# Kernel tuning notes

Measured on AMD Instinct MI355X. Metric: run time of the kernel, lower is better.

The kernel has to match this reference:

```python
import jax, jax.numpy as jnp
import numpy as np

B, S, TRG, SRC2 = 64, 2048, 512, 1024  # batch, src_len, trg_hidden, 2*src_hidden


def setup_inputs() -> dict:
    key = jax.random.key(0)
    ks = jax.random.split(key, 9)
    return {
        "dehy": jax.random.normal(ks[0], (B, TRG), dtype=jnp.float32),
        "enhy": jax.random.normal(ks[1], (B, S, SRC2), dtype=jnp.float32),
        "past_attn": jax.random.uniform(ks[2], (B, S), dtype=jnp.float32),
        "src_mask": jax.random.randint(ks[3], (B, S), 0, 2, dtype=jnp.int32),
        # parameters (torch Linear: y = x @ W.T + b)
        "W_en": jax.random.normal(ks[4], (TRG, SRC2), dtype=jnp.float32) * 0.02,
        "b_en": jnp.zeros((TRG,), dtype=jnp.float32),
        "W_de": jax.random.normal(ks[5], (TRG, TRG), dtype=jnp.float32) * 0.02,
        "w_cv": jax.random.normal(ks[6], (TRG,), dtype=jnp.float32) * 0.02,   # attn_cv_in: Linear(1, trg)
        "w_warp": jax.random.normal(ks[7], (TRG,), dtype=jnp.float32) * 0.02, # attn_warp_in: Linear(trg, 1)
    }


def reference(dehy, enhy, past_attn, src_mask, W_en, b_en, W_de, w_cv, w_warp):
    # luong_concat score with 'asee' coverage term
    # attn_agg: [B, S, TRG]
    attn_agg = (
        jnp.einsum("bsd,hd->bsh", enhy, W_en) + b_en
        + (dehy @ W_de.T)[:, None, :]
        + past_attn[..., None] * w_cv
    )
    attn_agg = jnp.tanh(attn_agg)
    attn_ee = jnp.einsum("bsh,h->bs", attn_agg, w_warp)  # [B, S]
    # masked_fill(|mask| == 0, -1e20)
    attn_ee = jnp.where(jnp.abs(src_mask) == 0, jnp.float32(-1e20), attn_ee)
    attn = jax.nn.softmax(attn_ee, axis=1)
    c_encoder = jnp.einsum("bs,bsd->bd", attn, enhy)  # [B, SRC2]
    return (c_encoder, attn, attn_ee)
```

## Files before the change

### kernel.cpp

```cpp
#include <hip/hip_runtime.h>
#include <hip/hip_bf16.h>

#define B_   64
#define S_   2048
#define TRG_ 512
#define K_   1024

typedef short short8 __attribute__((ext_vector_type(8)));
typedef short short4v __attribute__((ext_vector_type(4)));
typedef float f32x4  __attribute__((ext_vector_type(4)));
typedef unsigned short us4 __attribute__((ext_vector_type(4)));

__device__ __forceinline__ unsigned short f2bf(float f) {
    union { float f; unsigned int u; } v; v.f = f;
    unsigned int u = v.u;
    unsigned int r = (u + 0x7fffu + ((u >> 16) & 1u)) >> 16;
    return (unsigned short)r;
}

__device__ __forceinline__ short4v cvt4(f32x4 a) {
    union { __hip_bfloat162 h[2]; short4v v; } u;
    u.h[0] = __float22bfloat162_rn(float2{a[0], a[1]});
    u.h[1] = __float22bfloat162_rn(float2{a[2], a[3]});
    return u.v;
}

__global__ void wen_convert_kernel(const float* __restrict__ Wen,
                                   unsigned short* __restrict__ Wbf) {
    int idx = blockIdx.x * 256 + threadIdx.x;
    float4 f = ((const float4*)Wen)[idx];
    us4 o = { f2bf(f.x), f2bf(f.y), f2bf(f.z), f2bf(f.w) };
    ((us4*)Wbf)[idx] = o;
}

__global__ void deproj_kernel(const float* __restrict__ dehy,
                              const float* __restrict__ Wde,
                              const float* __restrict__ ben,
                              float* __restrict__ dp) {
    int b = blockIdx.x >> 1;
    int h = ((blockIdx.x & 1) << 8) + threadIdx.x;
    const float4* dv = (const float4*)(dehy + (size_t)b * TRG_);
    const float4* wv = (const float4*)(Wde + (size_t)h * TRG_);
    float s = ben[h];
    #pragma unroll 4
    for (int t = 0; t < TRG_ / 4; ++t) {
        float4 a = dv[t], w = wv[t];
        s += a.x * w.x + a.y * w.y + a.z * w.z + a.w * w.w;
    }
    dp[b * TRG_ + h] = s;
}

__global__ __launch_bounds__(512, 4) void score_kernel(
    const float* __restrict__ enhy,
    const unsigned short* __restrict__ Wbf,
    const float* __restrict__ dp,
    const float* __restrict__ past_attn,
    const int* __restrict__ src_mask,
    const float* __restrict__ w_cv,
    const float* __restrict__ w_warp,
    float* __restrict__ out_ee)
{
    __shared__ unsigned short Bbuf[512 * 32];
    __shared__ unsigned short Abuf[2][64 * 32];
    __shared__ float red[8][64];

    const int tid  = threadIdx.x;
    const int lane = tid & 63;
    const int w    = tid >> 6;
    const int lj   = lane & 15;
    const int lg   = lane >> 4;
    const int m0   = blockIdx.x * 64;
    const int b    = m0 >> 11;

    const int kx = ((lg ^ ((lj >> 1) & 3)) << 4);

    f32x4 acc[4][4];
    const f32x4 fz = {0.f, 0.f, 0.f, 0.f};
    #pragma unroll
    for (int i = 0; i < 4; ++i)
        #pragma unroll
        for (int j = 0; j < 4; ++j) acc[i][j] = fz;

    const int arow = tid >> 3;
    const int akq  = tid & 7;
    const float* aSrc = enhy + (size_t)(m0 + arow) * K_ + (akq << 2);
    const int aDstByte = arow * 64 + (((akq >> 1) ^ ((arow >> 1) & 3)) << 4) + ((akq & 1) << 3);

    const int brow0 = tid >> 2;
    const int bkc0  = tid & 3;
    const unsigned short* bSrc0 = Wbf + (size_t)brow0 * K_ + ((bkc0 ^ ((brow0 >> 1) & 3)) << 3);
    const int bDst0 = w * 1024;

#define LOADA(R, kt) { R = __builtin_nontemporal_load((const f32x4*)(aSrc + ((kt) << 5))); }
#define WRITEA(sel, R) { \
    *(short4v*)((char*)&Abuf[0][0] + (sel) * 4096 + aDstByte) = cvt4(R); }
#define STAGEB(kt) { \
    _Pragma("unroll") \
    for (int j_ = 0; j_ < 4; ++j_) { \
        __builtin_amdgcn_global_load_lds( \
            (const __attribute__((address_space(1))) void*)(bSrc0 + (size_t)j_ * 128 * K_ + ((kt) << 5)), \
            (__attribute__((address_space(3))) void*)((char*)&Bbuf[0] + bDst0 + j_ * 8192), \
            16, 0, 0); \
    } }
#define MIDBAR(N) \
    asm volatile("s_waitcnt vmcnt(" #N ") lgkmcnt(0)" ::: "memory"); \
    __builtin_amdgcn_sched_barrier(0); \
    __builtin_amdgcn_s_barrier(); \
    __builtin_amdgcn_sched_barrier(0);
#define ENDBAR() \
    asm volatile("s_waitcnt lgkmcnt(0)" ::: "memory"); \
    __builtin_amdgcn_sched_barrier(0); \
    __builtin_amdgcn_s_barrier(); \
    __builtin_amdgcn_sched_barrier(0);

    auto compute = [&](int sel) {
        const char* Bbase = (const char*)&Bbuf[0];
        const char* Abase = (const char*)&Abuf[0][0] + sel * 4096;
        short8 bfr[4];
        #pragma unroll
        for (int fn = 0; fn < 4; ++fn) {
            int r = (w << 6) + (fn << 4) + lj;
            bfr[fn] = *(const short8*)(Bbase + r * 64 + kx);
        }
        #pragma unroll
        for (int fm = 0; fm < 4; ++fm) {
            int rA = (fm << 4) + lj;
            short8 af = *(const short8*)(Abase + rA * 64 + kx);
            #pragma unroll
            for (int fn = 0; fn < 4; ++fn)
                acc[fm][fn] = __builtin_amdgcn_mfma_f32_16x16x32_bf16(af, bfr[fn], acc[fm][fn], 0, 0, 0);
        }
    };

    f32x4 aR0, aR1;
    LOADA(aR0, 0);
    LOADA(aR1, 1);
    WRITEA(0, aR0);

    for (int kt2 = 0; kt2 < 30; kt2 += 2) {
        STAGEB(kt2)
        WRITEA(1, aR1);
        LOADA(aR0, kt2 + 2);
        MIDBAR(1)
        compute(0);
        ENDBAR()
        STAGEB(kt2 + 1)
        WRITEA(0, aR0);
        LOADA(aR1, kt2 + 3);
        MIDBAR(1)
        compute(1);
        ENDBAR()
    }
    STAGEB(30)
    WRITEA(1, aR1);
    MIDBAR(0)
    compute(0);
    ENDBAR()
    STAGEB(31)
    MIDBAR(0)
    compute(1);

#undef LOADA
#undef WRITEA
#undef STAGEB
#undef MIDBAR
#undef ENDBAR

    float dep4[4], wcv4[4], wwp4[4];
    #pragma unroll
    for (int fn = 0; fn < 4; ++fn) {
        int h = (w << 6) + (fn << 4) + lj;
        dep4[fn] = dp[b * TRG_ + h];
        wcv4[fn] = w_cv[h];
        wwp4[fn] = w_warp[h];
    }
    #pragma unroll
    for (int fm = 0; fm < 4; ++fm) {
        #pragma unroll
        for (int reg = 0; reg < 4; ++reg) {
            int row = (fm << 4) + (lg << 2) + reg;
            float pa = past_attn[m0 + row];
            float p = 0.f;
            #pragma unroll
            for (int fn = 0; fn < 4; ++fn) {
                float v = acc[fm][fn][reg] + dep4[fn] + pa * wcv4[fn];
                float e = __expf(2.f * v);
                float t = 1.f - 2.f * __builtin_amdgcn_rcpf(e + 1.f);
                p += t * wwp4[fn];
            }
            p += __shfl_xor(p, 1);
            p += __shfl_xor(p, 2);
            p += __shfl_xor(p, 4);
            p += __shfl_xor(p, 8);
            if (lj == 0) red[w][row] = p;
        }
    }
    __syncthreads();
    if (tid < 64) {
        float ee = 0.f;
        #pragma unroll
        for (int ww = 0; ww < 8; ++ww) ee += red[ww][tid];
        int msk = src_mask[m0 + tid];
        if (msk == 0) ee = -1e20f;
        out_ee[m0 + tid] = ee;
    }
}

__global__ void softmax_kernel(const float* __restrict__ ee, float* __restrict__ attn) {
    int b = blockIdx.x, tid = threadIdx.x;
    const float* row = ee + (size_t)b * S_;
    float v[8]; float mx = -3.0e38f;
    #pragma unroll
    for (int i = 0; i < 8; ++i) { v[i] = row[tid + (i << 8)]; mx = fmaxf(mx, v[i]); }
    #pragma unroll
    for (int off = 32; off > 0; off >>= 1) mx = fmaxf(mx, __shfl_xor(mx, off));
    __shared__ float sred[4];
    int w = tid >> 6, lane = tid & 63;
    if (lane == 0) sred[w] = mx;
    __syncthreads();
    mx = fmaxf(fmaxf(sred[0], sred[1]), fmaxf(sred[2], sred[3]));
    float sum = 0.f;
    #pragma unroll
    for (int i = 0; i < 8; ++i) { v[i] = __expf(v[i] - mx); sum += v[i]; }
    #pragma unroll
    for (int off = 32; off > 0; off >>= 1) sum += __shfl_xor(sum, off);
    __syncthreads();
    if (lane == 0) sred[w] = sum;
    __syncthreads();
    sum = sred[0] + sred[1] + sred[2] + sred[3];
    float inv = 1.f / sum;
    float* orow = attn + (size_t)b * S_;
    #pragma unroll
    for (int i = 0; i < 8; ++i) orow[tid + (i << 8)] = v[i] * inv;
}

__global__ void ctx_partial_kernel(const float* __restrict__ attn,
                                   const float* __restrict__ enhy,
                                   float* __restrict__ part) {
    int bx = blockIdx.x;
    int b = bx >> 5, sc = bx & 31;
    int tid = threadIdx.x;
    const float4* e4 = (const float4*)(enhy + ((size_t)b * S_ + sc * 64) * K_);
    const float* ar = attn + (size_t)b * S_ + sc * 64;
    float4 acc = {0.f, 0.f, 0.f, 0.f};
    #pragma unroll 8
    for (int s = 0; s < 64; ++s) {
        float a = ar[s];
        float4 ev = e4[(size_t)s * 256 + tid];
        acc.x += a * ev.x; acc.y += a * ev.y; acc.z += a * ev.z; acc.w += a * ev.w;
    }
    ((float4*)part)[(size_t)(sc * 64 + b) * 256 + tid] = acc;
}

__global__ void ctx_reduce_kernel(const float* __restrict__ part, float* __restrict__ outc) {
    int idx = blockIdx.x * 256 + threadIdx.x;
    int b = idx >> 10, d = idx & 1023;
    float s = 0.f;
    #pragma unroll
    for (int sc = 0; sc < 32; ++sc) s += part[(size_t)((sc << 6) + b) * 1024 + d];
    outc[idx] = s;
}

extern "C" void kernel_launch(void* const* d_in, const int* in_sizes, int n_in,
                              void* d_out, int out_size, void* d_ws, size_t ws_size,
                              hipStream_t stream) {
    (void)in_sizes; (void)n_in; (void)out_size; (void)ws_size;

    const float* dehy = (const float*)d_in[0];
    const float* enhy = (const float*)d_in[1];
    const float* past = (const float*)d_in[2];
    const int*   mask = (const int*)d_in[3];
    const float* Wen  = (const float*)d_in[4];
    const float* ben  = (const float*)d_in[5];
    const float* Wde  = (const float*)d_in[6];
    const float* wcv  = (const float*)d_in[7];
    const float* wwp  = (const float*)d_in[8];

    float* out      = (float*)d_out;
    float* out_c    = out;
    float* out_attn = out + 65536;
    float* out_ee   = out + 65536 + 131072;

    char* ws = (char*)d_ws;
    unsigned short* Wbf = (unsigned short*)ws;
    float* dp   = (float*)(ws + (1 << 20));
    float* part = (float*)(ws + (1 << 20) + (1 << 17));

    wen_convert_kernel<<<512, 256, 0, stream>>>(Wen, Wbf);
    deproj_kernel<<<128, 256, 0, stream>>>(dehy, Wde, ben, dp);
    score_kernel<<<2048, 512, 0, stream>>>(enhy, Wbf, dp, past, mask, wcv, wwp, out_ee);
    softmax_kernel<<<64, 256, 0, stream>>>(out_ee, out_attn);
    ctx_partial_kernel<<<2048, 256, 0, stream>>>(out_attn, enhy, part);
    ctx_reduce_kernel<<<256, 256, 0, stream>>>(part, out_c);
}
```

Baseline: 365.0 us.

## Fuse softmax normalization into context kernel and pin load/store scheduling order

The softmax kernel is reduced to computing per-row max and reciprocal sum. Each context-partial block now recomputes its 64 attention weights from the scores, writes them to the attn output and keeps them in shared memory, which removes one full write-then-read pass over attn. Separately, sched_barriers are added between the B staging, A writes and A loads in the score GEMM loop to stop the compiler from reordering them. The trade-off is an extra syncthreads and exp per context block, and a more rigid instruction schedule in the GEMM.

```diff
diff --git a/kernel.cpp b/kernel.cpp
--- a/kernel.cpp
+++ b/kernel.cpp
@@ -91,6 +91,7 @@
     const unsigned short* bSrc0 = Wbf + (size_t)brow0 * K_ + ((bkc0 ^ ((brow0 >> 1) & 3)) << 3);
     const int bDst0 = w * 1024;
 
+#define SB0() __builtin_amdgcn_sched_barrier(0);
 #define LOADA(R, kt) { R = __builtin_nontemporal_load((const f32x4*)(aSrc + ((kt) << 5))); }
 #define WRITEA(sel, R) { \
     *(short4v*)((char*)&Abuf[0][0] + (sel) * 4096 + aDstByte) = cvt4(R); }
@@ -104,14 +105,10 @@
     } }
 #define MIDBAR(N) \
     asm volatile("s_waitcnt vmcnt(" #N ") lgkmcnt(0)" ::: "memory"); \
-    __builtin_amdgcn_sched_barrier(0); \
-    __builtin_amdgcn_s_barrier(); \
-    __builtin_amdgcn_sched_barrier(0);
+    SB0() __builtin_amdgcn_s_barrier(); SB0()
 #define ENDBAR() \
     asm volatile("s_waitcnt lgkmcnt(0)" ::: "memory"); \
-    __builtin_amdgcn_sched_barrier(0); \
-    __builtin_amdgcn_s_barrier(); \
-    __builtin_amdgcn_sched_barrier(0);
+    SB0() __builtin_amdgcn_s_barrier(); SB0()
 
     auto compute = [&](int sel) {
         const char* Bbase = (const char*)&Bbuf[0];
@@ -136,30 +133,32 @@
     LOADA(aR0, 0);
     LOADA(aR1, 1);
     WRITEA(0, aR0);
+    SB0()
 
     for (int kt2 = 0; kt2 < 30; kt2 += 2) {
-        STAGEB(kt2)
-        WRITEA(1, aR1);
-        LOADA(aR0, kt2 + 2);
+        STAGEB(kt2) SB0()
+        WRITEA(1, aR1); SB0()
+        LOADA(aR0, kt2 + 2); SB0()
         MIDBAR(1)
         compute(0);
         ENDBAR()
-        STAGEB(kt2 + 1)
-        WRITEA(0, aR0);
-        LOADA(aR1, kt2 + 3);
+        STAGEB(kt2 + 1) SB0()
+        WRITEA(0, aR0); SB0()
+        LOADA(aR1, kt2 + 3); SB0()
         MIDBAR(1)
         compute(1);
         ENDBAR()
     }
-    STAGEB(30)
-    WRITEA(1, aR1);
+    STAGEB(30) SB0()
+    WRITEA(1, aR1); SB0()
     MIDBAR(0)
     compute(0);
     ENDBAR()
-    STAGEB(31)
+    STAGEB(31) SB0()
     MIDBAR(0)
     compute(1);
 
+#undef SB0
 #undef LOADA
 #undef WRITEA
 #undef STAGEB
@@ -206,7 +205,7 @@
     }
 }
 
-__global__ void softmax_kernel(const float* __restrict__ ee, float* __restrict__ attn) {
+__global__ void rowstat_kernel(const float* __restrict__ ee, float2* __restrict__ mxinv) {
     int b = blockIdx.x, tid = threadIdx.x;
     const float* row = ee + (size_t)b * S_;
     float v[8]; float mx = -3.0e38f;
@@ -221,31 +220,37 @@
     mx = fmaxf(fmaxf(sred[0], sred[1]), fmaxf(sred[2], sred[3]));
     float sum = 0.f;
     #pragma unroll
-    for (int i = 0; i < 8; ++i) { v[i] = __expf(v[i] - mx); sum += v[i]; }
+    for (int i = 0; i < 8; ++i) sum += __expf(v[i] - mx);
     #pragma unroll
     for (int off = 32; off > 0; off >>= 1) sum += __shfl_xor(sum, off);
     __syncthreads();
     if (lane == 0) sred[w] = sum;
     __syncthreads();
     sum = sred[0] + sred[1] + sred[2] + sred[3];
-    float inv = 1.f / sum;
-    float* orow = attn + (size_t)b * S_;
-    #pragma unroll
-    for (int i = 0; i < 8; ++i) orow[tid + (i << 8)] = v[i] * inv;
-}
-
-__global__ void ctx_partial_kernel(const float* __restrict__ attn,
+    if (tid == 0) mxinv[b] = float2{mx, 1.f / sum};
+}
+
+__global__ void ctx_partial_kernel(const float* __restrict__ ee,
+                                   const float2* __restrict__ mxinv,
                                    const float* __restrict__ enhy,
+                                   float* __restrict__ attn,
                                    float* __restrict__ part) {
+    __shared__ float a_sh[64];
     int bx = blockIdx.x;
     int b = bx >> 5, sc = bx & 31;
     int tid = threadIdx.x;
+    float2 mi = mxinv[b];
+    if (tid < 64) {
+        float a = __expf(ee[(size_t)b * S_ + sc * 64 + tid] - mi.x) * mi.y;
+        a_sh[tid] = a;
+        attn[(size_t)b * S_ + sc * 64 + tid] = a;
+    }
+    __syncthreads();
     const float4* e4 = (const float4*)(enhy + ((size_t)b * S_ + sc * 64) * K_);
-    const float* ar = attn + (size_t)b * S_ + sc * 64;
     float4 acc = {0.f, 0.f, 0.f, 0.f};
     #pragma unroll 8
     for (int s = 0; s < 64; ++s) {
-        float a = ar[s];
+        float a = a_sh[s];
         float4 ev = e4[(size_t)s * 256 + tid];
         acc.x += a * ev.x; acc.y += a * ev.y; acc.z += a * ev.z; acc.w += a * ev.w;
     }
@@ -283,13 +288,14 @@
 
     char* ws = (char*)d_ws;
     unsigned short* Wbf = (unsigned short*)ws;
-    float* dp   = (float*)(ws + (1 << 20));
-    float* part = (float*)(ws + (1 << 20) + (1 << 17));
+    float* dp    = (float*)(ws + (1 << 20));
+    float* part  = (float*)(ws + (1 << 20) + (1 << 17));
+    float2* mxiv = (float2*)(ws + (size_t)10 * (1 << 20));
 
     wen_convert_kernel<<<512, 256, 0, stream>>>(Wen, Wbf);
     deproj_kernel<<<128, 256, 0, stream>>>(dehy, Wde, ben, dp);
     score_kernel<<<2048, 512, 0, stream>>>(enhy, Wbf, dp, past, mask, wcv, wwp, out_ee);
-    softmax_kernel<<<64, 256, 0, stream>>>(out_ee, out_attn);
-    ctx_partial_kernel<<<2048, 256, 0, stream>>>(out_attn, enhy, part);
+    rowstat_kernel<<<64, 256, 0, stream>>>(out_ee, mxiv);
+    ctx_partial_kernel<<<2048, 256, 0, stream>>>(out_ee, mxiv, enhy, out_attn, part);
     ctx_reduce_kernel<<<256, 256, 0, stream>>>(part, out_c);
 }
```

Result: faster. 339.7 us (-6.9%).
